# Performance work log

Hardware: AMD Instinct MI355X
Metric: run time of the kernel (lower is better)

The kernel has to match this reference:

```python
import jax, jax.numpy as jnp
import numpy as np

N_GRAPHS = 256
GRADES = jnp.array([0, 1, 1, 1, 2, 2, 2, 3])      # blade -> grade for Cl(3,0): [1,e1,e2,e3,e12,e13,e23,e123]
G_ONEHOT = jnp.eye(4)[GRADES]                      # (8,4) blade->grade one-hot
NUM_RBF, CUTOFF, NEG_SLOPE = 20, 10.0, 0.2
HID, HEADS, HD, LAYERS = 64, 4, 16, 4
EPS_LN = 1e-6


def _mv_linear_sub(x, w, b):
    # MVLinear with per-grade weights. x:(N,I,8), w:(4,O,I), b:(O,) added to scalar blade.
    wb = w[GRADES]                                 # (8,O,I)
    out = jnp.einsum('nib,boi->nob', x, wb)
    return out.at[..., 0].add(b)


def _gat_layer(h, src, dst, edge_scalar, pw, pb, asrc, adst, wsrc, wdst):
    N = h.shape[0]
    z = _mv_linear_sub(h, pw, pb).reshape(N, HEADS, HD, 8)
    # fold per-grade importance weights into per-blade contraction vectors
    a_s = asrc * wsrc[:, GRADES][:, None, :]       # (H,C,8)
    a_d = adst * wdst[:, GRADES][:, None, :]
    s_src = jnp.einsum('nhcb,hcb->nh', z, a_s)
    s_dst = jnp.einsum('nhcb,hcb->nh', z, a_d)
    e = jax.nn.leaky_relu(s_src[src] + s_dst[dst] + edge_scalar, NEG_SLOPE)  # (E,H)
    e_max = jax.ops.segment_max(e, dst, num_segments=N)
    alpha = jnp.exp(e - e_max[dst])
    a_sum = jax.ops.segment_sum(alpha, dst, num_segments=N)
    alpha = alpha / (a_sum[dst] + 1e-16)
    out = jax.ops.segment_sum(z[src] * alpha[:, :, None, None], dst, num_segments=N)
    return out.reshape(N, HEADS * HD, 8)


def _mv_silu(x, a, b):
    # x:(N,C,8); a,b:(C,4). Gate by scalar part (grade 0) and per-grade squared magnitudes.
    qg = jnp.einsum('ncb,bg->ncg', x * x, G_ONEHOT)                 # (N,C,4) mag2 per grade
    norms = jnp.concatenate([x[..., :1], qg[..., 1:]], axis=-1)     # (N,C,4)
    gate = jax.nn.sigmoid(a * norms + b)[..., GRADES]               # (N,C,8)
    return gate * x


def _mv_layernorm(x, a):
    n = jnp.sqrt(jnp.sum(x * x, axis=-1))                           # (N,C)
    n = jnp.mean(n, axis=1, keepdims=True) + EPS_LN                 # (N,1)
    return a[None, :, None] * x / n[..., None]


def _forward(floats, z, edge_index, batch):
    (pos, atom_w, inw, inb, ew1, eb1, ew2, eb2,
     proj_w, proj_b, a_src, a_dst, w_src, w_dst,
     ln_a, silu_a, silu_b, ppw, ppb, pw1, pb1, pw2, pb2) = floats
    src, dst = edge_index[0], edge_index[1]
    N = pos.shape[0]

    # RBF edge features -> per-head scalar bias
    d2 = jnp.sum((pos[src] - pos[dst]) ** 2, axis=-1)
    dist = jnp.where(d2 > 0, jnp.sqrt(jnp.where(d2 > 0, d2, 1.0)), 0.0)
    centers = jnp.linspace(0.0, CUTOFF, NUM_RBF)
    width = CUTOFF / (NUM_RBF - 1)
    rbf = jnp.exp(-0.5 * ((dist[:, None] - centers) / width) ** 2)  # (E,20)
    edge_scalar = jax.nn.silu(rbf @ ew1.T + eb1) @ ew2.T + eb2      # (E,H)

    # node multivector embedding: scalars from atom embedding, grade-1 from centered positions
    h_sca = jnp.zeros((N, HID, 8), dtype=pos.dtype).at[..., 0].set(atom_w[z])
    cnt = jax.ops.segment_sum(jnp.ones((N,), pos.dtype), batch, num_segments=N_GRAPHS)
    pos_mean = jax.ops.segment_sum(pos, batch, num_segments=N_GRAPHS) / jnp.maximum(cnt, 1.0)[:, None]
    pos_c = pos - pos_mean[batch]
    h_vec = jnp.zeros((N, 1, 8), dtype=pos.dtype).at[:, 0, 1:4].set(pos_c)
    h = jnp.concatenate([h_sca, h_vec], axis=1)                     # (N,HID+1,8)
    h = jnp.einsum('nib,oi->nob', h, inw).at[..., 0].add(inb)       # input_proj, subspaces=False

    for l in range(LAYERS):
        h_res = h
        h = _gat_layer(h, src, dst, edge_scalar, proj_w[l], proj_b[l],
                       a_src[l], a_dst[l], w_src[l], w_dst[l])
        h = _mv_silu(h, silu_a[l], silu_b[l])
        h = h + h_res
        h = _mv_layernorm(h, ln_a[l])

    h = _mv_linear_sub(h, ppw, ppb)[..., 0]                         # (N,HID) scalar blade
    g = jax.ops.segment_sum(h, batch, num_segments=N_GRAPHS)        # 'add' readout -> (B,HID)
    out = jax.nn.silu(g @ pw1.T + pb1) @ pw2.T + pb2                # (B,1)
    return out[:, 0]


def setup_inputs() -> dict:
    key = jax.random.key(0)
    ks = jax.random.split(key, 24)
    N, E, B = 20000, 320000, N_GRAPHS
    rn = lambda k, shape, s=0.1: jax.random.normal(k, shape, jnp.float32) * s
    return dict(
        pos=jax.random.normal(ks[0], (N, 3), jnp.float32) * 3.0,
        z=jax.random.randint(ks[1], (N,), 0, 100),
        edge_index=jax.random.randint(ks[2], (2, E), 0, N),
        batch=jnp.sort(jax.random.randint(ks[3], (N,), 0, B)),
        atom_embed_w=rn(ks[4], (100, HID)),
        inproj_w=rn(ks[5], (HID, HID + 1)),
        inproj_b=rn(ks[6], (HID,)),
        edge_w1=rn(ks[7], (HID, NUM_RBF)),
        edge_b1=rn(ks[8], (HID,)),
        edge_w2=rn(ks[9], (HEADS, HID)),
        edge_b2=rn(ks[10], (HEADS,)),
        proj_w=rn(ks[11], (LAYERS, 4, HID, HID)),
        proj_b=rn(ks[12], (LAYERS, HID)),
        a_src=rn(ks[13], (LAYERS, HEADS, HD, 8)),
        a_dst=rn(ks[14], (LAYERS, HEADS, HD, 8)),
        w_src=jnp.ones((LAYERS, HEADS, 4), jnp.float32),
        w_dst=jnp.ones((LAYERS, HEADS, 4), jnp.float32),
        ln_a=jnp.ones((LAYERS, HID), jnp.float32),
        silu_a=jnp.ones((LAYERS, HID, 4), jnp.float32),
        silu_b=jnp.zeros((LAYERS, HID, 4), jnp.float32),
        prepool_w=rn(ks[15], (4, HID, HID)),
        prepool_b=rn(ks[16], (HID,)),
        post_w1=rn(ks[17], (HID, HID)),
        post_b1=rn(ks[18], (HID,)),
        post_w2=rn(ks[19], (1, HID)),
        post_b2=rn(ks[20], (1,)),
    )


def reference(pos, z, edge_index, batch, atom_embed_w, inproj_w, inproj_b,
              edge_w1, edge_b1, edge_w2, edge_b2, proj_w, proj_b,
              a_src, a_dst, w_src, w_dst, ln_a, silu_a, silu_b,
              prepool_w, prepool_b, post_w1, post_b1, post_w2, post_b2):
    floats = (pos, atom_embed_w, inproj_w, inproj_b, edge_w1, edge_b1, edge_w2, edge_b2,
              proj_w, proj_b, a_src, a_dst, w_src, w_dst,
              ln_a, silu_a, silu_b, prepool_w, prepool_b, post_w1, post_b1, post_w2, post_b2)
    return _forward(floats, z, edge_index, batch)
```

## Files before the change

kernel.cpp:

```cpp
#include <hip/hip_runtime.h>
#include <hip/hip_bf16.h>
#include <math.h>

#define HID 64
#define HEADS 4
#define LAYERS 4
#define NRBF 20
#define NG 256
#define CB 512
#define HSTRIDE 68
#define CAPB 64
#define TABN 8192
#define NATOM 100

typedef __attribute__((ext_vector_type(8))) short short8;
typedef __attribute__((ext_vector_type(4))) float floatx4;

__device__ __forceinline__ int gradeOf(int b){ return (b==0)?0:((b<4)?1:((b<7)?2:3)); }
__device__ __forceinline__ unsigned short f2bf(float f){
    __hip_bfloat16 h = __float2bfloat16(f);
    return *(unsigned short*)&h;
}
__device__ __forceinline__ float bflo(int u){ return __uint_as_float(((unsigned)u)<<16); }
__device__ __forceinline__ float bfhi(int u){ return __uint_as_float(((unsigned)u)&0xFFFF0000u); }

struct P {
    const float *pos; const int *zidx; const int *ei; const int *batch;
    const float *atom_w, *inproj_w, *inproj_b, *ew1, *eb1, *ew2, *eb2;
    const float *proj_w, *proj_b, *a_src, *a_dst, *w_src, *w_dst;
    const float *ln_a, *silu_a, *silu_b, *ppw, *ppb, *pw1, *pb1, *pw2, *pb2;
    float *out;
    int *counts; float *possum; float *pcnt; float *gbuf;
    int *bucket;
    float *escb;
    float *tab;
    unsigned short *WTbf; float *ppw0T; float *w1T; float *sbf;
    float *embT;
    unsigned short *hb;
    unsigned short *zA; unsigned short *zB;
    float *ssA; float *sdA; float *ssB; float *sdB;
    int N, E, Mtiles;
};

__global__ __launch_bounds__(256) void k1_kernel(P p){
    const int PREP_TOTAL = LAYERS*4*64*64 + 2*HID*HID + 2*LAYERS*HEADS;
    const int CP = (PREP_TOTAL+255)/256;
    const int CN = (p.N+255)/256;
    const int CT = (TABN+1+3)/4;
    int bid = blockIdx.x, t = threadIdx.x;
    if (bid < CP){
        int idx = bid*256 + t;
        const int szW = LAYERS*4*64*64;
        const int e2 = szW + HID*HID;
        const int e3 = e2 + HID*HID;
        if (idx < szW){
            p.WTbf[idx] = f2bf(p.proj_w[idx]);
        } else if (idx < e2){
            int r = idx - szW; int i = r/HID, o = r%HID;
            p.ppw0T[r] = p.ppw[o*HID + i];
        } else if (idx < e3){
            int r = idx - e2; int i = r/HID, o = r%HID;
            p.w1T[r] = p.pw1[o*HID + i];
        } else if (idx < e3 + 2*LAYERS*HEADS){
            int r = idx - e3;
            int hh = r & 3; int type = (r>>2)&1; int l = r>>3;
            const float* a = type ? p.a_dst : p.a_src;
            const float* w = type ? p.w_dst : p.w_src;
            float wh = w[l*16 + hh*4 + 0];
            float s = 0.f;
            for (int c=0;c<16;c++)
                s += a[l*512 + (hh*16+c)*8 + 0] * wh * p.proj_b[l*64 + hh*16 + c];
            p.sbf[r] = s;
        }
    } else if (bid < CP+CN){
        int n = (bid-CP)*256 + t;
        if (n < p.N){
            int g = p.batch[n];
            atomicAdd(&p.possum[g*3+0], p.pos[n*3+0]);
            atomicAdd(&p.possum[g*3+1], p.pos[n*3+1]);
            atomicAdd(&p.possum[g*3+2], p.pos[n*3+2]);
            atomicAdd(&p.pcnt[g], 1.0f);
        }
    } else if (bid < CP+CN+CT){
        int wv = t>>6, lane = t&63;
        int i = (bid-CP-CN)*4 + wv;
        if (i > TABN) return;
        float d = (float)i * (16.0f/TABN);
        float t0 = d * (19.0f/10.0f);
        float hv = p.eb1[lane];
        #pragma unroll
        for (int k=0;k<NRBF;k++){
            float a = t0 - (float)k;
            hv += __expf(-0.5f*a*a) * p.ew1[lane*NRBF+k];
        }
        float act = hv/(1.0f+__expf(-hv));
        float p0 = act*p.ew2[0*HID+lane];
        float p1 = act*p.ew2[1*HID+lane];
        float p2 = act*p.ew2[2*HID+lane];
        float p3 = act*p.ew2[3*HID+lane];
        #pragma unroll
        for (int off=1; off<64; off<<=1){
            p0 += __shfl_xor(p0,off,64);
            p1 += __shfl_xor(p1,off,64);
            p2 += __shfl_xor(p2,off,64);
            p3 += __shfl_xor(p3,off,64);
        }
        if (lane==0){
            *(float4*)&p.tab[(size_t)i*4] = make_float4(p0+p.eb2[0], p1+p.eb2[1],
                                                        p2+p.eb2[2], p3+p.eb2[3]);
        }
    } else {
        int wv = t>>6, lane = t&63;
        int za = (bid-CP-CN-CT)*4 + wv;
        if (za >= NATOM) return;
        float accv = p.inproj_b[lane];
        for (int i=0;i<HID;i++)
            accv += p.atom_w[(size_t)za*HID + i] * p.inproj_w[lane*65 + i];
        p.embT[(size_t)za*HID + lane] = accv;
    }
}

__device__ __forceinline__ void proj_core(const P& p, int pl, int n0, int nt, int lane,
        const short8* afr, bool rows16,
        unsigned short* zout, float* ssout, float* sdout){
    const unsigned short* WTl = p.WTbf + (size_t)pl*4*64*64;
    const float* pbl = p.proj_b + pl*HID;
    const float* a_src_l = p.a_src + pl*512;
    const float* a_dst_l = p.a_dst + pl*512;
    const float* w_src_l = p.w_src + pl*16;
    const float* w_dst_l = p.w_dst + pl*16;
    const float* sb_l = p.sbf + pl*8;
    int m = lane&15, quad = lane>>4;
    int o = nt*16 + m;
    float cs[4][2][4];
    float pss[4], psd[4];
    #pragma unroll
    for (int r=0;r<4;r++){ pss[r]=0.f; psd[r]=0.f; }
    #pragma unroll
    for (int bp=0; bp<4; bp++){
        const int b0 = 2*bp, b1 = b0+1;
        const int g0 = gradeOf(b0), g1 = gradeOf(b1);
        const short8 w00 = *(const short8*)(WTl + (g0*64 + o)*64 + quad*8);
        const short8 w01 = *(const short8*)(WTl + (g0*64 + o)*64 + 32 + quad*8);
        short8 w10, w11;
        if (g1==g0){ w10 = w00; w11 = w01; }
        else {
            w10 = *(const short8*)(WTl + (g1*64 + o)*64 + quad*8);
            w11 = *(const short8*)(WTl + (g1*64 + o)*64 + 32 + quad*8);
        }
        floatx4 c0 = {0.f,0.f,0.f,0.f}, c1 = {0.f,0.f,0.f,0.f};
        c0 = __builtin_amdgcn_mfma_f32_16x16x32_bf16(afr[4*bp+0], w00, c0, 0,0,0);
        c0 = __builtin_amdgcn_mfma_f32_16x16x32_bf16(afr[4*bp+1], w01, c0, 0,0,0);
        c1 = __builtin_amdgcn_mfma_f32_16x16x32_bf16(afr[4*bp+2], w10, c1, 0,0,0);
        c1 = __builtin_amdgcn_mfma_f32_16x16x32_bf16(afr[4*bp+3], w11, c1, 0,0,0);
        float as0 = a_src_l[o*8+b0]*w_src_l[nt*4+g0];
        float as1 = a_src_l[o*8+b1]*w_src_l[nt*4+g1];
        float ad0 = a_dst_l[o*8+b0]*w_dst_l[nt*4+g0];
        float ad1 = a_dst_l[o*8+b1]*w_dst_l[nt*4+g1];
        float bias0 = (bp==0) ? pbl[o] : 0.0f;
        #pragma unroll
        for (int r=0;r<4;r++){
            float v0 = c0[r], v1 = c1[r];
            pss[r] += v0*as0 + v1*as1;
            psd[r] += v0*ad0 + v1*ad1;
            cs[bp][0][r] = v0 + bias0;
            cs[bp][1][r] = v1;
        }
    }
    #pragma unroll
    for (int r=0;r<4;r++){
        int row = quad*4 + r;
        bool rowok = rows16 ? true : (quad==0);
        int nn = n0 + (rows16 ? row : r);
        if (rowok && nn < p.N){
            unsigned short pk[8];
            #pragma unroll
            for (int bp=0;bp<4;bp++){
                pk[2*bp]   = f2bf(cs[bp][0][r]);
                pk[2*bp+1] = f2bf(cs[bp][1][r]);
            }
            *(int4*)(zout + (size_t)nn*CB + o*8) = *(int4*)pk;
        }
    }
    #pragma unroll
    for (int r=0;r<4;r++){
        float vs = pss[r], vd = psd[r];
        #pragma unroll
        for (int off=1; off<16; off<<=1){
            vs += __shfl_xor(vs, off, 64);
            vd += __shfl_xor(vd, off, 64);
        }
        int row = quad*4 + r;
        bool rowok = rows16 ? true : (quad==0);
        int nn = n0 + (rows16 ? row : r);
        if (m==0 && rowok && nn<p.N){
            ssout[nn*4+nt] = vs + sb_l[nt];
            sdout[nn*4+nt] = vd + sb_l[4+nt];
        }
    }
}

__global__ __launch_bounds__(256) void k2_kernel(P p){
    __shared__ unsigned short hAl[8*16*HSTRIDE];
    int t = threadIdx.x, wv = t>>6, lane = t&63;
    if ((int)blockIdx.x >= p.Mtiles){
        int e = ((int)blockIdx.x - p.Mtiles)*256 + t;
        if (e >= p.E) return;
        int s = p.ei[e], d = p.ei[p.E+e];
        float dx = p.pos[s*3+0]-p.pos[d*3+0];
        float dy = p.pos[s*3+1]-p.pos[d*3+1];
        float dz = p.pos[s*3+2]-p.pos[d*3+2];
        float dist = sqrtf(dx*dx+dy*dy+dz*dz);
        float idxf = fminf(dist * ((float)TABN/16.0f), (float)(TABN-1));
        int i0 = (int)idxf;
        float fr = idxf - (float)i0;
        float4 f0 = *(const float4*)&p.tab[(size_t)i0*4];
        float4 f1 = *(const float4*)&p.tab[(size_t)(i0+1)*4];
        float4 escv = make_float4(
            f0.x + (f1.x-f0.x)*fr, f0.y + (f1.y-f0.y)*fr,
            f0.z + (f1.z-f0.z)*fr, f0.w + (f1.w-f0.w)*fr);
        int slot = atomicAdd(&p.counts[d],1);
        if (slot < CAPB){
            p.bucket[(size_t)d*CAPB + slot] = s;
            *(float4*)&p.escb[((size_t)d*CAPB + slot)*4] = escv;
        }
        return;
    }
    int n0 = blockIdx.x*16;
    float wvv = p.inproj_w[lane*65 + 64];
    for (int k=0;k<4;k++){
        int m = wv*4 + k;
        int n = n0 + m;
        if (n < p.N){
            int zn = p.zidx[n];
            float acc = p.embT[(size_t)zn*HID + lane];
            int g = p.batch[n];
            float cm = p.pcnt[g]; cm = cm>1.0f?cm:1.0f;
            float px = p.pos[n*3+0]-p.possum[g*3+0]/cm;
            float py = p.pos[n*3+1]-p.possum[g*3+1]/cm;
            float pz = p.pos[n*3+2]-p.possum[g*3+2]/cm;
            unsigned short pk[8];
            pk[0]=f2bf(acc); pk[1]=f2bf(wvv*px); pk[2]=f2bf(wvv*py); pk[3]=f2bf(wvv*pz);
            pk[4]=0; pk[5]=0; pk[6]=0; pk[7]=0;
            *(int4*)(p.hb + (size_t)n*CB + lane*8) = *(int4*)pk;
            #pragma unroll
            for (int b=0;b<8;b++) hAl[(b*16+m)*HSTRIDE + lane] = pk[b];
        } else {
            #pragma unroll
            for (int b=0;b<8;b++) hAl[(b*16+m)*HSTRIDE + lane] = 0;
        }
    }
    __syncthreads();
    int m = lane&15, quad = lane>>4;
    short8 afr[16];
    #pragma unroll
    for (int bp=0;bp<4;bp++){
        int b0=2*bp, b1=b0+1;
        afr[4*bp+0] = *(const short8*)(hAl + (b0*16+m)*HSTRIDE + quad*8);
        afr[4*bp+1] = *(const short8*)(hAl + (b0*16+m)*HSTRIDE + 32 + quad*8);
        afr[4*bp+2] = *(const short8*)(hAl + (b1*16+m)*HSTRIDE + quad*8);
        afr[4*bp+3] = *(const short8*)(hAl + (b1*16+m)*HSTRIDE + 32 + quad*8);
    }
    proj_core(p, 0, n0, wv, lane, afr, true, p.zA, p.ssA, p.sdA);
}

__device__ __forceinline__ void fmab8(const float* lwv, int h_id, int J,
                                      const int4* zv, float* acc, float& dn){
    #pragma unroll
    for (int i=0;i<8;i++){
        float w = lwv[(J+i)*4 + h_id];
        acc[0] += w*bflo(zv[i].x); acc[1] += w*bfhi(zv[i].x);
        acc[2] += w*bflo(zv[i].y); acc[3] += w*bfhi(zv[i].y);
        acc[4] += w*bflo(zv[i].z); acc[5] += w*bfhi(zv[i].z);
        acc[6] += w*bflo(zv[i].w); acc[7] += w*bfhi(zv[i].w);
        dn += w;
    }
}

__global__ __launch_bounds__(256) void agg_kernel(P p, int l,
        const unsigned short* __restrict__ zin, const float* __restrict__ ssin,
        const float* __restrict__ sdin, int last){
    __shared__ float lw[4][256];
    int wv = threadIdx.x>>6, lane = threadIdx.x&63;
    int n = blockIdx.x*4 + wv;
    if (n >= p.N) return;
    float* lwv = lw[wv];
    int4 hres = *((const int4*)(p.hb + (size_t)n*CB) + lane);
    float4 sdl = *(const float4*)&sdin[n*4];
    int deg = min(p.counts[n], CAPB);
    int h_id = lane>>4;
    const int* bs = p.bucket + (size_t)n*CAPB;
    int s = 0;
    float l0=-1e30f,l1=-1e30f,l2=-1e30f,l3=-1e30f;
    if (lane < deg){
        s = bs[lane];
        float4 evv = *(const float4*)&p.escb[((size_t)n*CAPB + lane)*4];
        float4 sv  = *(const float4*)&ssin[s*4];
        l0 = sv.x+sdl.x+evv.x; l0=(l0>=0.f)?l0:0.2f*l0;
        l1 = sv.y+sdl.y+evv.y; l1=(l1>=0.f)?l1:0.2f*l1;
        l2 = sv.z+sdl.z+evv.z; l2=(l2>=0.f)?l2:0.2f*l2;
        l3 = sv.w+sdl.w+evv.w; l3=(l3>=0.f)?l3:0.2f*l3;
    }
    int bc = (deg+7)>>3;
    int4 zv[8];
    if (bc>0){
        #pragma unroll
        for (int i=0;i<8;i++){
            int sb = __builtin_amdgcn_readlane(s, i);
            zv[i] = *((const int4*)(zin + (size_t)(unsigned)sb*CB) + lane);
        }
    }
    float m0=l0,m1=l1,m2=l2,m3=l3;
    #pragma unroll
    for (int off=1; off<64; off<<=1){
        m0=fmaxf(m0,__shfl_xor(m0,off,64));
        m1=fmaxf(m1,__shfl_xor(m1,off,64));
        m2=fmaxf(m2,__shfl_xor(m2,off,64));
        m3=fmaxf(m3,__shfl_xor(m3,off,64));
    }
    *(float4*)&lwv[lane*4] = make_float4(__expf(l0-m0),__expf(l1-m1),
                                         __expf(l2-m2),__expf(l3-m3));
    float acc[8];
    #pragma unroll
    for (int k=0;k<8;k++) acc[k]=0.f;
    float dn = 0.f;
    if (bc>0) fmab8(lwv, h_id, 0, zv, acc, dn);
    for (int j=8; j<bc*8; j+=8){
        #pragma unroll
        for (int i=0;i<8;i++){
            int sb = __builtin_amdgcn_readlane(s, j+i);
            zv[i] = *((const int4*)(zin + (size_t)(unsigned)sb*CB) + lane);
        }
        fmab8(lwv, h_id, j, zv, acc, dn);
    }
    float inv = 1.0f/(dn + 1e-16f);
    float x[8];
    #pragma unroll
    for (int k=0;k<8;k++) x[k] = acc[k]*inv;
    const float* silu_a_l = p.silu_a + l*HID*4;
    const float* silu_b_l = p.silu_b + l*HID*4;
    float4 sa = *(const float4*)&silu_a_l[lane*4];
    float4 sb = *(const float4*)&silu_b_l[lane*4];
    float n1 = x[1]*x[1]+x[2]*x[2]+x[3]*x[3];
    float n2 = x[4]*x[4]+x[5]*x[5]+x[6]*x[6];
    float n3 = x[7]*x[7];
    float g0 = 1.0f/(1.0f+__expf(-(sa.x*x[0]+sb.x)));
    float g1 = 1.0f/(1.0f+__expf(-(sa.y*n1+sb.y)));
    float g2 = 1.0f/(1.0f+__expf(-(sa.z*n2+sb.z)));
    float g3 = 1.0f/(1.0f+__expf(-(sa.w*n3+sb.w)));
    float val[8];
    val[0]=g0*x[0]+bflo(hres.x); val[1]=g1*x[1]+bfhi(hres.x);
    val[2]=g1*x[2]+bflo(hres.y); val[3]=g1*x[3]+bfhi(hres.y);
    val[4]=g2*x[4]+bflo(hres.z); val[5]=g2*x[5]+bfhi(hres.z);
    val[6]=g2*x[6]+bflo(hres.w); val[7]=g3*x[7]+bfhi(hres.w);
    float ssq=0.f;
    #pragma unroll
    for (int k=0;k<8;k++) ssq += val[k]*val[k];
    float nr = sqrtf(ssq);
    #pragma unroll
    for (int off=1; off<64; off<<=1) nr += __shfl_xor(nr, off, 64);
    float mean = nr*(1.0f/64.0f) + 1e-6f;
    float scale = p.ln_a[l*HID + lane]/mean;
    float outv[8];
    #pragma unroll
    for (int k=0;k<8;k++) outv[k] = scale*val[k];
    if (!last){
        unsigned short pk[8];
        #pragma unroll
        for (int k=0;k<8;k++) pk[k] = f2bf(outv[k]);
        *(int4*)(p.hb + (size_t)n*CB + lane*8) = *(int4*)pk;
    } else {
        float x0 = outv[0];
        float accp = p.ppb[lane];
        for (int i=0;i<HID;i++) accp += __shfl(x0, i, 64) * p.ppw0T[i*HID + lane];
        atomicAdd(&p.gbuf[p.batch[n]*HID + lane], accp);
    }
}

__global__ __launch_bounds__(256) void proj_kernel(P p, int pl,
        unsigned short* zout, float* ssout, float* sdout){
    __shared__ unsigned short hAl[8*16*HSTRIDE];
    int t = threadIdx.x, wv = t>>6, lane = t&63;
    int n0 = blockIdx.x*16;
    for (int k=0;k<4;k++){
        int m = wv*4 + k;
        int n = n0 + m;
        if (n < p.N){
            int4 hv = *((const int4*)(p.hb + (size_t)n*CB) + lane);
            unsigned short* pk = (unsigned short*)&hv;
            #pragma unroll
            for (int b=0;b<8;b++) hAl[(b*16+m)*HSTRIDE + lane] = pk[b];
        } else {
            #pragma unroll
            for (int b=0;b<8;b++) hAl[(b*16+m)*HSTRIDE + lane] = 0;
        }
    }
    __syncthreads();
    int m = lane&15, quad = lane>>4;
    short8 afr[16];
    #pragma unroll
    for (int bp=0;bp<4;bp++){
        int b0=2*bp, b1=b0+1;
        afr[4*bp+0] = *(const short8*)(hAl + (b0*16+m)*HSTRIDE + quad*8);
        afr[4*bp+1] = *(const short8*)(hAl + (b0*16+m)*HSTRIDE + 32 + quad*8);
        afr[4*bp+2] = *(const short8*)(hAl + (b1*16+m)*HSTRIDE + quad*8);
        afr[4*bp+3] = *(const short8*)(hAl + (b1*16+m)*HSTRIDE + 32 + quad*8);
    }
    proj_core(p, pl, n0, wv, lane, afr, true, zout, ssout, sdout);
}

__global__ void final_kernel(P p){
    int gid = blockIdx.x; int o = threadIdx.x;
    float gv = p.gbuf[gid*HID + o];
    float a = p.pb1[o];
    for (int i=0;i<HID;i++) a += __shfl(gv, i, 64) * p.w1T[i*HID + o];
    float act = a/(1.0f+__expf(-a));
    float pv = act * p.pw2[o];
    #pragma unroll
    for (int off=1; off<64; off<<=1) pv += __shfl_xor(pv, off, 64);
    if (o==0) p.out[gid] = pv + p.pb2[0];
}

extern "C" void kernel_launch(void* const* d_in, const int* in_sizes, int n_in,
                              void* d_out, int out_size, void* d_ws, size_t ws_size,
                              hipStream_t stream) {
    P p;
    p.pos      = (const float*)d_in[0];
    p.zidx     = (const int*)  d_in[1];
    p.ei       = (const int*)  d_in[2];
    p.batch    = (const int*)  d_in[3];
    p.atom_w   = (const float*)d_in[4];
    p.inproj_w = (const float*)d_in[5];
    p.inproj_b = (const float*)d_in[6];
    p.ew1      = (const float*)d_in[7];
    p.eb1      = (const float*)d_in[8];
    p.ew2      = (const float*)d_in[9];
    p.eb2      = (const float*)d_in[10];
    p.proj_w   = (const float*)d_in[11];
    p.proj_b   = (const float*)d_in[12];
    p.a_src    = (const float*)d_in[13];
    p.a_dst    = (const float*)d_in[14];
    p.w_src    = (const float*)d_in[15];
    p.w_dst    = (const float*)d_in[16];
    p.ln_a     = (const float*)d_in[17];
    p.silu_a   = (const float*)d_in[18];
    p.silu_b   = (const float*)d_in[19];
    p.ppw      = (const float*)d_in[20];
    p.ppb      = (const float*)d_in[21];
    p.pw1      = (const float*)d_in[22];
    p.pb1      = (const float*)d_in[23];
    p.pw2      = (const float*)d_in[24];
    p.pb2      = (const float*)d_in[25];
    p.out = (float*)d_out;

    const int N = in_sizes[0]/3;
    const int E = in_sizes[2]/2;
    p.N = N; p.E = E; p.Mtiles = (N+15)/16;

    float* wsf = (float*)d_ws;
    size_t off = 0;
    auto alloc = [&](size_t nelem){ size_t r = off; off += (nelem + 63) & ~(size_t)63; return r; };
    size_t o_counts = alloc(N);
    size_t o_possum = alloc(NG*3);
    size_t o_pcnt   = alloc(NG);
    size_t o_g      = alloc(NG*HID);
    size_t zero_end = off;
    size_t o_bucket = alloc((size_t)N*CAPB);
    size_t o_escb   = alloc((size_t)N*CAPB*4);
    size_t o_tab    = alloc((size_t)(TABN+2)*4);
    size_t o_ssA    = alloc((size_t)N*4);
    size_t o_sdA    = alloc((size_t)N*4);
    size_t o_ssB    = alloc((size_t)N*4);
    size_t o_sdB    = alloc((size_t)N*4);
    size_t o_WTbf   = alloc((size_t)LAYERS*4*64*64/2);
    size_t o_ppw0T  = alloc(HID*HID);
    size_t o_w1T    = alloc(HID*HID);
    size_t o_sbf    = alloc(2*LAYERS*HEADS);
    size_t o_embT   = alloc((size_t)NATOM*HID);
    size_t o_hb     = alloc((size_t)N*CB/2);
    size_t o_zA     = alloc((size_t)N*CB/2);
    size_t o_zB     = alloc((size_t)N*CB/2);

    p.counts = (int*)(wsf + o_counts);
    p.possum = wsf + o_possum;
    p.pcnt   = wsf + o_pcnt;
    p.gbuf   = wsf + o_g;
    p.bucket = (int*)(wsf + o_bucket);
    p.escb   = wsf + o_escb;
    p.tab    = wsf + o_tab;
    p.ssA    = wsf + o_ssA;
    p.sdA    = wsf + o_sdA;
    p.ssB    = wsf + o_ssB;
    p.sdB    = wsf + o_sdB;
    p.WTbf   = (unsigned short*)(wsf + o_WTbf);
    p.ppw0T  = wsf + o_ppw0T;
    p.w1T    = wsf + o_w1T;
    p.sbf    = wsf + o_sbf;
    p.embT   = wsf + o_embT;
    p.hb     = (unsigned short*)(wsf + o_hb);
    p.zA     = (unsigned short*)(wsf + o_zA);
    p.zB     = (unsigned short*)(wsf + o_zB);

    hipMemsetAsync(wsf, 0, zero_end*sizeof(float), stream);

    const int PREP_TOTAL = LAYERS*4*64*64 + 2*HID*HID + 2*LAYERS*HEADS;
    const int CP = (PREP_TOTAL+255)/256;
    const int CN = (N+255)/256;
    const int CE = (E+255)/256;
    const int CT = (TABN+1+3)/4;
    const int CEMB = (NATOM+3)/4;

    k1_kernel<<<CP+CN+CT+CEMB, 256, 0, stream>>>(p);
    k2_kernel<<<p.Mtiles + CE, 256, 0, stream>>>(p);

    const int AG = (N+3)/4;
    agg_kernel <<<AG,       256, 0, stream>>>(p, 0, p.zA, p.ssA, p.sdA, 0);
    proj_kernel<<<p.Mtiles, 256, 0, stream>>>(p, 1, p.zB, p.ssB, p.sdB);
    agg_kernel <<<AG,       256, 0, stream>>>(p, 1, p.zB, p.ssB, p.sdB, 0);
    proj_kernel<<<p.Mtiles, 256, 0, stream>>>(p, 2, p.zA, p.ssA, p.sdA);
    agg_kernel <<<AG,       256, 0, stream>>>(p, 2, p.zA, p.ssA, p.sdA, 0);
    proj_kernel<<<p.Mtiles, 256, 0, stream>>>(p, 3, p.zB, p.ssB, p.sdB);
    agg_kernel <<<AG,       256, 0, stream>>>(p, 3, p.zB, p.ssB, p.sdB, 1);

    final_kernel<<<NG, 64, 0, stream>>>(p);
}
```

Baseline: 446.6 us.

## Pack edge scalars to bf16, defer pre-pool linear, widen proj blocks

Edge attention scalars are now stored as packed bf16 pairs (8 bytes per edge instead of 16), which halves the escb traffic in the edge-build and aggregation kernels at some cost in precision. The last layer's per-node pre-pool linear (a 64-step shuffle matvec per node) is replaced by an atomic sum of the raw scalar features per graph. The linear map and count-scaled bias are then applied once per graph in final_kernel, relying on linearity. proj_kernel now processes two 16-node tiles per 512-thread block, using eight waves and a double-size shared buffer.

Result: no change. 448.1 us (+0.3%).

```diff
diff --git a/kernel.cpp b/kernel.cpp
--- a/kernel.cpp
+++ b/kernel.cpp
@@ -23,6 +23,9 @@
 }
 __device__ __forceinline__ float bflo(int u){ return __uint_as_float(((unsigned)u)<<16); }
 __device__ __forceinline__ float bfhi(int u){ return __uint_as_float(((unsigned)u)&0xFFFF0000u); }
+__device__ __forceinline__ int packbf2(float a, float b){
+    return (int)f2bf(a) | ((int)f2bf(b)<<16);
+}
 
 struct P {
     const float *pos; const int *zidx; const int *ei; const int *batch;
@@ -32,7 +35,7 @@
     float *out;
     int *counts; float *possum; float *pcnt; float *gbuf;
     int *bucket;
-    float *escb;
+    int *escb;
     float *tab;
     unsigned short *WTbf; float *ppw0T; float *w1T; float *sbf;
     float *embT;
@@ -216,13 +219,13 @@
         float fr = idxf - (float)i0;
         float4 f0 = *(const float4*)&p.tab[(size_t)i0*4];
         float4 f1 = *(const float4*)&p.tab[(size_t)(i0+1)*4];
-        float4 escv = make_float4(
-            f0.x + (f1.x-f0.x)*fr, f0.y + (f1.y-f0.y)*fr,
-            f0.z + (f1.z-f0.z)*fr, f0.w + (f1.w-f0.w)*fr);
         int slot = atomicAdd(&p.counts[d],1);
         if (slot < CAPB){
             p.bucket[(size_t)d*CAPB + slot] = s;
-            *(float4*)&p.escb[((size_t)d*CAPB + slot)*4] = escv;
+            int2 epk = make_int2(
+                packbf2(f0.x + (f1.x-f0.x)*fr, f0.y + (f1.y-f0.y)*fr),
+                packbf2(f0.z + (f1.z-f0.z)*fr, f0.w + (f1.w-f0.w)*fr));
+            *(int2*)&p.escb[((size_t)d*CAPB + slot)*2] = epk;
         }
         return;
     }
@@ -294,12 +297,12 @@
     float l0=-1e30f,l1=-1e30f,l2=-1e30f,l3=-1e30f;
     if (lane < deg){
         s = bs[lane];
-        float4 evv = *(const float4*)&p.escb[((size_t)n*CAPB + lane)*4];
+        int2 ev = *((const int2*)p.escb + ((size_t)n*CAPB + lane));
         float4 sv  = *(const float4*)&ssin[s*4];
-        l0 = sv.x+sdl.x+evv.x; l0=(l0>=0.f)?l0:0.2f*l0;
-        l1 = sv.y+sdl.y+evv.y; l1=(l1>=0.f)?l1:0.2f*l1;
-        l2 = sv.z+sdl.z+evv.z; l2=(l2>=0.f)?l2:0.2f*l2;
-        l3 = sv.w+sdl.w+evv.w; l3=(l3>=0.f)?l3:0.2f*l3;
+        l0 = sv.x+sdl.x+bflo(ev.x); l0=(l0>=0.f)?l0:0.2f*l0;
+        l1 = sv.y+sdl.y+bfhi(ev.x); l1=(l1>=0.f)?l1:0.2f*l1;
+        l2 = sv.z+sdl.z+bflo(ev.y); l2=(l2>=0.f)?l2:0.2f*l2;
+        l3 = sv.w+sdl.w+bfhi(ev.y); l3=(l3>=0.f)?l3:0.2f*l3;
     }
     int bc = (deg+7)>>3;
     int4 zv[8];
@@ -370,50 +373,54 @@
         for (int k=0;k<8;k++) pk[k] = f2bf(outv[k]);
         *(int4*)(p.hb + (size_t)n*CB + lane*8) = *(int4*)pk;
     } else {
-        float x0 = outv[0];
-        float accp = p.ppb[lane];
-        for (int i=0;i<HID;i++) accp += __shfl(x0, i, 64) * p.ppw0T[i*HID + lane];
-        atomicAdd(&p.gbuf[p.batch[n]*HID + lane], accp);
-    }
-}
-
-__global__ __launch_bounds__(256) void proj_kernel(P p, int pl,
+        atomicAdd(&p.gbuf[p.batch[n]*HID + lane], outv[0]);
+    }
+}
+
+__global__ __launch_bounds__(512) void proj_kernel(P p, int pl,
         unsigned short* zout, float* ssout, float* sdout){
-    __shared__ unsigned short hAl[8*16*HSTRIDE];
+    __shared__ unsigned short hAl[2][8*16*HSTRIDE];
     int t = threadIdx.x, wv = t>>6, lane = t&63;
-    int n0 = blockIdx.x*16;
+    int nb = blockIdx.x*32;
     for (int k=0;k<4;k++){
-        int m = wv*4 + k;
-        int n = n0 + m;
+        int m2 = wv*4 + k;
+        int tile = m2>>4, mr = m2&15;
+        int n = nb + m2;
         if (n < p.N){
             int4 hv = *((const int4*)(p.hb + (size_t)n*CB) + lane);
             unsigned short* pk = (unsigned short*)&hv;
             #pragma unroll
-            for (int b=0;b<8;b++) hAl[(b*16+m)*HSTRIDE + lane] = pk[b];
+            for (int b=0;b<8;b++) hAl[tile][(b*16+mr)*HSTRIDE + lane] = pk[b];
         } else {
             #pragma unroll
-            for (int b=0;b<8;b++) hAl[(b*16+m)*HSTRIDE + lane] = 0;
+            for (int b=0;b<8;b++) hAl[tile][(b*16+mr)*HSTRIDE + lane] = 0;
         }
     }
     __syncthreads();
+    int tile = wv>>2, nt = wv&3;
+    int n0 = nb + tile*16;
+    const unsigned short* hT = hAl[tile];
     int m = lane&15, quad = lane>>4;
     short8 afr[16];
     #pragma unroll
     for (int bp=0;bp<4;bp++){
         int b0=2*bp, b1=b0+1;
-        afr[4*bp+0] = *(const short8*)(hAl + (b0*16+m)*HSTRIDE + quad*8);
-        afr[4*bp+1] = *(const short8*)(hAl + (b0*16+m)*HSTRIDE + 32 + quad*8);
-        afr[4*bp+2] = *(const short8*)(hAl + (b1*16+m)*HSTRIDE + quad*8);
-        afr[4*bp+3] = *(const short8*)(hAl + (b1*16+m)*HSTRIDE + 32 + quad*8);
-    }
-    proj_core(p, pl, n0, wv, lane, afr, true, zout, ssout, sdout);
+        afr[4*bp+0] = *(const short8*)(hT + (b0*16+m)*HSTRIDE + quad*8);
+        afr[4*bp+1] = *(const short8*)(hT + (b0*16+m)*HSTRIDE + 32 + quad*8);
+        afr[4*bp+2] = *(const short8*)(hT + (b1*16+m)*HSTRIDE + quad*8);
+        afr[4*bp+3] = *(const short8*)(hT + (b1*16+m)*HSTRIDE + 32 + quad*8);
+    }
+    proj_core(p, pl, n0, nt, lane, afr, true, zout, ssout, sdout);
 }
 
 __global__ void final_kernel(P p){
     int gid = blockIdx.x; int o = threadIdx.x;
-    float gv = p.gbuf[gid*HID + o];
+    float gs = p.gbuf[gid*HID + o];
+    float cnt = p.pcnt[gid];
+    float gsc = cnt * p.ppb[o];
+    for (int i=0;i<HID;i++) gsc += __shfl(gs, i, 64) * p.ppw0T[i*HID + o];
     float a = p.pb1[o];
-    for (int i=0;i<HID;i++) a += __shfl(gv, i, 64) * p.w1T[i*HID + o];
+    for (int i=0;i<HID;i++) a += __shfl(gsc, i, 64) * p.w1T[i*HID + o];
     float act = a/(1.0f+__expf(-a));
     float pv = act * p.pw2[o];
     #pragma unroll
@@ -466,7 +473,7 @@
     size_t o_g      = alloc(NG*HID);
     size_t zero_end = off;
     size_t o_bucket = alloc((size_t)N*CAPB);
-    size_t o_escb   = alloc((size_t)N*CAPB*4);
+    size_t o_escb   = alloc((size_t)N*CAPB*2);
     size_t o_tab    = alloc((size_t)(TABN+2)*4);
     size_t o_ssA    = alloc((size_t)N*4);
     size_t o_sdA    = alloc((size_t)N*4);
@@ -486,7 +493,7 @@
     p.pcnt   = wsf + o_pcnt;
     p.gbuf   = wsf + o_g;
     p.bucket = (int*)(wsf + o_bucket);
-    p.escb   = wsf + o_escb;
+    p.escb   = (int*)(wsf + o_escb);
     p.tab    = wsf + o_tab;
     p.ssA    = wsf + o_ssA;
     p.sdA    = wsf + o_sdA;
@@ -514,13 +521,14 @@
     k2_kernel<<<p.Mtiles + CE, 256, 0, stream>>>(p);
 
     const int AG = (N+3)/4;
-    agg_kernel <<<AG,       256, 0, stream>>>(p, 0, p.zA, p.ssA, p.sdA, 0);
-    proj_kernel<<<p.Mtiles, 256, 0, stream>>>(p, 1, p.zB, p.ssB, p.sdB);
-    agg_kernel <<<AG,       256, 0, stream>>>(p, 1, p.zB, p.ssB, p.sdB, 0);
-    proj_kernel<<<p.Mtiles, 256, 0, stream>>>(p, 2, p.zA, p.ssA, p.sdA);
-    agg_kernel <<<AG,       256, 0, stream>>>(p, 2, p.zA, p.ssA, p.sdA, 0);
-    proj_kernel<<<p.Mtiles, 256, 0, stream>>>(p, 3, p.zB, p.ssB, p.sdB);
-    agg_kernel <<<AG,       256, 0, stream>>>(p, 3, p.zB, p.ssB, p.sdB, 1);
+    const int PG = (N+31)/32;
+    agg_kernel <<<AG, 256, 0, stream>>>(p, 0, p.zA, p.ssA, p.sdA, 0);
+    proj_kernel<<<PG, 512, 0, stream>>>(p, 1, p.zB, p.ssB, p.sdB);
+    agg_kernel <<<AG, 256, 0, stream>>>(p, 1, p.zB, p.ssB, p.sdB, 0);
+    proj_kernel<<<PG, 512, 0, stream>>>(p, 2, p.zA, p.ssA, p.sdA);
+    agg_kernel <<<AG, 256, 0, stream>>>(p, 2, p.zA, p.ssA, p.sdA, 0);
+    proj_kernel<<<PG, 512, 0, stream>>>(p, 3, p.zB, p.ssB, p.sdB);
+    agg_kernel <<<AG, 256, 0, stream>>>(p, 3, p.zB, p.ssB, p.sdB, 1);
 
     final_kernel<<<NG, 64, 0, stream>>>(p);
 }
```
